# Kernel tuning notes

Measured on AMD Instinct MI355X. Metric: run time of the kernel, lower is better.

The kernel has to match this reference:

```python
import jax, jax.numpy as jnp
import numpy as np

N_NODES = 100000
N_EDGES = 3200000
N_GRAPHS = 64
IN_FEATS = 128
NUM_CLASSES = 10


def setup_inputs() -> dict:
    key = jax.random.key(0)
    ks = jax.random.split(key, 12)
    in_feat = jax.random.normal(ks[0], (N_NODES, IN_FEATS), dtype=jnp.float32)
    src = jax.random.randint(ks[1], (N_EDGES,), 0, N_NODES, dtype=jnp.int32)
    dst = jax.random.randint(ks[2], (N_EDGES,), 0, N_NODES, dtype=jnp.int32)
    graph_ids = jnp.sort(jax.random.randint(ks[3], (N_NODES,), 0, N_GRAPHS, dtype=jnp.int32))
    def glorot(k, fan_in, fan_out):
        s = jnp.sqrt(6.0 / (fan_in + fan_out))
        return jax.random.uniform(k, (fan_in, fan_out), jnp.float32, -s, s)
    W1 = glorot(ks[4], IN_FEATS, 64); b1 = jnp.zeros((64,), jnp.float32)
    W2 = glorot(ks[5], 64, 128);      b2 = jnp.zeros((128,), jnp.float32)
    W3 = glorot(ks[6], 128, 64);      b3 = jnp.zeros((64,), jnp.float32)
    Wd = glorot(ks[7], 64, NUM_CLASSES)
    bd = jnp.zeros((NUM_CLASSES,), jnp.float32)
    return {"in_feat": in_feat, "src": src, "dst": dst, "graph_ids": graph_ids,
            "W1": W1, "b1": b1, "W2": W2, "b2": b2, "W3": W3, "b3": b3,
            "Wd": Wd, "bd": bd}


def _graph_conv(h, src, dst, norm_src, norm_dst, W, b):
    # DGL GraphConv, norm='both': h' = D_in^{-1/2} A (D_out^{-1/2} h) W + b
    x = h * norm_src[:, None]
    m = jax.ops.segment_sum(x[src], dst, num_segments=N_NODES)
    m = m * norm_dst[:, None]
    return m @ W + b


def reference(in_feat, src, dst, graph_ids, W1, b1, W2, b2, W3, b3, Wd, bd):
    ones = jnp.ones((N_EDGES,), jnp.float32)
    deg_out = jax.ops.segment_sum(ones, src, num_segments=N_NODES)
    deg_in = jax.ops.segment_sum(ones, dst, num_segments=N_NODES)
    norm_src = jax.lax.rsqrt(jnp.clip(deg_out, 1.0))
    norm_dst = jax.lax.rsqrt(jnp.clip(deg_in, 1.0))

    h = jax.nn.relu(_graph_conv(in_feat, src, dst, norm_src, norm_dst, W1, b1))
    h = jax.nn.relu(_graph_conv(h, src, dst, norm_src, norm_dst, W2, b2))
    h = jax.nn.relu(_graph_conv(h, src, dst, norm_src, norm_dst, W3, b3))

    hg = jax.ops.segment_sum(h, graph_ids, num_segments=N_GRAPHS)  # [G, 64]
    hg = jnp.tanh(hg)
    return hg @ Wd + bd  # [G, num_classes]
```

## Files before the change

kernel.cpp:

```cpp
#include <hip/hip_runtime.h>
#include <hip/hip_bf16.h>


constexpr int NN = 100000;
constexpr int NE = 3200000;
constexpr int NG = 64;

constexpr int CBITS = 16;
constexpr int CHUNK = 1 << CBITS;
constexpr int NCHUNK = (NE + CHUNK - 1) / CHUNK;
constexpr int WORDS4 = NN / 8;

typedef __attribute__((ext_vector_type(8))) short short8;
typedef __attribute__((ext_vector_type(4))) float f32x4;
typedef __attribute__((ext_vector_type(2))) float f32x2;


__global__ __launch_bounds__(1024) void hist_kernel(
    const int* __restrict__ src, const int* __restrict__ dst,
    uint* __restrict__ pdst, uint* __restrict__ psrc,
    unsigned char* __restrict__ lrank) {
  __shared__ uint bins[WORDS4];
  for (int i = threadIdx.x; i < WORDS4; i += 1024) bins[i] = 0;
  __syncthreads();
  const int c = blockIdx.x;
  const int start = c << CBITS;
  const int end = min(start + CHUNK, NE);
  if (blockIdx.y == 0) {
    for (int i = start + threadIdx.x; i < end; i += 1024) {
      int n = dst[i];
      uint old = atomicAdd(&bins[n >> 3], 1u << ((n & 7) * 4));
      lrank[i] = (unsigned char)((old >> ((n & 7) * 4)) & 0xf);
    }
  } else {
    for (int i = start + threadIdx.x; i < end; i += 1024) {
      int n = src[i];
      atomicAdd(&bins[n >> 3], 1u << ((n & 7) * 4));
    }
  }
  __syncthreads();
  uint* pp = ((blockIdx.y == 0) ? pdst : psrc) + (size_t)c * WORDS4;
  for (int i = threadIdx.x; i < WORDS4; i += 1024) pp[i] = bins[i];
}


__global__ __launch_bounds__(256) void reduce2_kernel(
    const uint* __restrict__ pdst, const uint* __restrict__ psrc,
    unsigned char* __restrict__ Pb, int* __restrict__ deg_in,
    float* __restrict__ nd, float* __restrict__ ns, float* __restrict__ hg) {
  int w = blockIdx.x * 256 + threadIdx.x;
  uint run[8] = {0, 0, 0, 0, 0, 0, 0, 0};
  if (blockIdx.y == 0) {
    if (w >= WORDS4) return;
#pragma unroll 7
    for (int c = 0; c < NCHUNK; ++c) {
      uint lo = run[0] | (run[1] << 8) | (run[2] << 16) | (run[3] << 24);
      uint hi = run[4] | (run[5] << 8) | (run[6] << 16) | (run[7] << 24);
      ((uint2*)(Pb + (size_t)c * NN))[w] = make_uint2(lo, hi);
      uint v = pdst[(size_t)c * WORDS4 + w];
#pragma unroll
      for (int k = 0; k < 8; ++k) run[k] += (v >> (4 * k)) & 0xfu;
    }
    ((int4*)deg_in)[2 * w] = make_int4(run[0], run[1], run[2], run[3]);
    ((int4*)deg_in)[2 * w + 1] = make_int4(run[4], run[5], run[6], run[7]);
    float4 f0, f1;
    f0.x = rsqrtf(fmaxf((float)run[0], 1.f));
    f0.y = rsqrtf(fmaxf((float)run[1], 1.f));
    f0.z = rsqrtf(fmaxf((float)run[2], 1.f));
    f0.w = rsqrtf(fmaxf((float)run[3], 1.f));
    f1.x = rsqrtf(fmaxf((float)run[4], 1.f));
    f1.y = rsqrtf(fmaxf((float)run[5], 1.f));
    f1.z = rsqrtf(fmaxf((float)run[6], 1.f));
    f1.w = rsqrtf(fmaxf((float)run[7], 1.f));
    ((float4*)nd)[2 * w] = f0;
    ((float4*)nd)[2 * w + 1] = f1;
  } else {
    if (blockIdx.x == 0) {
      for (int k = threadIdx.x; k < 1024; k += 256)
        ((float4*)hg)[k] = make_float4(0.f, 0.f, 0.f, 0.f);
    }
    if (w >= WORDS4) return;
#pragma unroll 7
    for (int c = 0; c < NCHUNK; ++c) {
      uint v = psrc[(size_t)c * WORDS4 + w];
#pragma unroll
      for (int k = 0; k < 8; ++k) run[k] += (v >> (4 * k)) & 0xfu;
    }
    float4 f0, f1;
    f0.x = rsqrtf(fmaxf((float)run[0], 1.f));
    f0.y = rsqrtf(fmaxf((float)run[1], 1.f));
    f0.z = rsqrtf(fmaxf((float)run[2], 1.f));
    f0.w = rsqrtf(fmaxf((float)run[3], 1.f));
    f1.x = rsqrtf(fmaxf((float)run[4], 1.f));
    f1.y = rsqrtf(fmaxf((float)run[5], 1.f));
    f1.z = rsqrtf(fmaxf((float)run[6], 1.f));
    f1.w = rsqrtf(fmaxf((float)run[7], 1.f));
    ((float4*)ns)[2 * w] = f0;
    ((float4*)ns)[2 * w + 1] = f1;
  }
}


__device__ __forceinline__ uint pack_bf16(float a, float b) {
  uint ua = __float_as_uint(a), ub = __float_as_uint(b);
  ua = (ua + 0x7fffu + ((ua >> 16) & 1u)) >> 16;
  ub = (ub + 0x7fffu + ((ub >> 16) & 1u)) & 0xffff0000u;
  return ua | ub;
}

__device__ __forceinline__ ushort to_bf16(float a) {
  uint ua = __float_as_uint(a);
  return (ushort)((ua + 0x7fffu + ((ua >> 16) & 1u)) >> 16);
}

union U16 {
  uint4 u;
  short8 s;
};
__device__ __forceinline__ short8 as_short8(uint4 u) {
  U16 t;
  t.u = u;
  return t.s;
}

__device__ __forceinline__ f32x2 bf2(uint u) {
  f32x2 r;
  r.x = __uint_as_float(u << 16);
  r.y = __uint_as_float(u & 0xffff0000u);
  return r;
}

__device__ __forceinline__ void add8(f32x2* a, uint4 v) {
  a[0] += bf2(v.x);
  a[1] += bf2(v.y);
  a[2] += bf2(v.z);
  a[3] += bf2(v.w);
}


__global__ __launch_bounds__(256) void scan1t_kernel(
    const int* __restrict__ deg, int* __restrict__ row_off,
    int* __restrict__ bsums, int n, const float* __restrict__ W1,
    const float* __restrict__ W2, const float* __restrict__ W3,
    ushort* __restrict__ Wt1, ushort* __restrict__ Wt2,
    ushort* __restrict__ Wt3) {
  int gi = blockIdx.x * 256 + threadIdx.x;
  if (gi < 8192) {
    int nn = gi >> 7, k = gi & 127;
    Wt1[gi] = to_bf16(W1[k * 64 + nn]);
  } else if (gi < 16384) {
    int j = gi - 8192;
    int nn = j >> 6, k = j & 63;
    Wt2[j] = to_bf16(W2[k * 128 + nn]);
  } else if (gi < 24576) {
    int j = gi - 16384;
    int nn = j >> 7, k = j & 127;
    Wt3[j] = to_bf16(W3[k * 64 + nn]);
  }
  __shared__ int s[256];
  int t = threadIdx.x;
  int base = blockIdx.x * 1024 + t * 4;
  int v0 = 0, v1 = 0, v2 = 0, v3 = 0;
  if (base + 0 < n) v0 = deg[base + 0];
  if (base + 1 < n) v1 = deg[base + 1];
  if (base + 2 < n) v2 = deg[base + 2];
  if (base + 3 < n) v3 = deg[base + 3];
  int sum = v0 + v1 + v2 + v3;
  s[t] = sum;
  __syncthreads();
  for (int off = 1; off < 256; off <<= 1) {
    int x = (t >= off) ? s[t - off] : 0;
    __syncthreads();
    s[t] += x;
    __syncthreads();
  }
  int excl = s[t] - sum;
  if (t == 255) bsums[blockIdx.x] = s[255];
  if (base + 0 < n) row_off[base + 0] = excl;
  if (base + 1 < n) row_off[base + 1] = excl + v0;
  if (base + 2 < n) row_off[base + 2] = excl + v0 + v1;
  if (base + 3 < n) row_off[base + 3] = excl + v0 + v1 + v2;
}


__global__ __launch_bounds__(256) void scan23_kernel(
    int* __restrict__ row_off, const int* __restrict__ bsums, int nb, int n) {
  __shared__ int si[128], so[128];
  int t = threadIdx.x;
  if (t < 128) {
    int v = (t < nb) ? bsums[t] : 0;
    si[t] = v;
    so[t] = v;
  }
  __syncthreads();
  for (int off = 1; off < 128; off <<= 1) {
    int x = 0;
    if (t < 128 && t >= off) x = si[t - off];
    __syncthreads();
    if (t < 128) si[t] += x;
    __syncthreads();
  }
  int i = blockIdx.x * 256 + t;
  if (i < n) {
    int bk = i >> 10;
    row_off[i] += si[bk] - so[bk];
  }
  if (blockIdx.x == 0 && t == 0) row_off[n] = si[127];
}


__global__ __launch_bounds__(256) void fillg1_kernel(
    const int* __restrict__ src, const int* __restrict__ dst,
    const int* __restrict__ row_off, const unsigned char* __restrict__ Pb,
    const unsigned char* __restrict__ lrank, int* __restrict__ csr, int e,
    const float* __restrict__ A, const ushort* __restrict__ Wt,
    const float* __restrict__ scale, ushort* __restrict__ C, int n,
    int gblocks) {
  if (blockIdx.x < (uint)gblocks) {
    int wid = threadIdx.x >> 6, lane = threadIdx.x & 63;
    int r = lane & 15, quad = lane >> 4;
    int m16 = blockIdx.x * 64 + wid * 16;
    if (m16 >= n) return;
    int mc = min(m16 + r, n - 1);
    short8 a[4];
#pragma unroll
    for (int ks = 0; ks < 4; ++ks) {
      const float4* p =
          (const float4*)(A + (size_t)mc * 128 + ks * 32 + quad * 8);
      float4 x = p[0], y = p[1];
      uint4 u;
      u.x = pack_bf16(x.x, x.y);
      u.y = pack_bf16(x.z, x.w);
      u.z = pack_bf16(y.x, y.y);
      u.w = pack_bf16(y.z, y.w);
      a[ks] = as_short8(u);
    }
#pragma unroll
    for (int nt = 0; nt < 4; ++nt) {
      f32x4 acc = {0.f, 0.f, 0.f, 0.f};
#pragma unroll
      for (int ks = 0; ks < 4; ++ks) {
        short8 b = as_short8(*(const uint4*)(Wt + (size_t)(nt * 16 + r) * 128 +
                                             ks * 32 + quad * 8));
        acc = __builtin_amdgcn_mfma_f32_16x16x32_bf16(a[ks], b, acc, 0, 0, 0);
      }
#pragma unroll
      for (int reg = 0; reg < 4; ++reg) {
        int m = m16 + quad * 4 + reg;
        if (m < n)
          C[(size_t)m * 64 + nt * 16 + r] = to_bf16(acc[reg] * scale[m]);
      }
    }
  } else {
    int i = (blockIdx.x - gblocks) * 256 + threadIdx.x;
    if (i < e) {
      int d = dst[i];
      int c = i >> CBITS;
      int pos = row_off[d] + (int)Pb[(size_t)c * NN + d] + (int)lrank[i];
      csr[pos] = src[i];
    }
  }
}


__global__ __launch_bounds__(256) void gemm23_kernel(
    const ushort* __restrict__ m2, const ushort* __restrict__ Wt2,
    const float* __restrict__ b2, const float* __restrict__ ns,
    const ushort* __restrict__ Wt3, ushort* __restrict__ t3, int n) {
  __shared__ ushort sX[4][16][136];
  int wid = threadIdx.x >> 6, lane = threadIdx.x & 63;
  int r = lane & 15, quad = lane >> 4;
  int m16 = blockIdx.x * 64 + wid * 16;
  if (m16 >= n) return;
  int mc = min(m16 + r, n - 1);
  short8 a1[2];
#pragma unroll
  for (int ks = 0; ks < 2; ++ks)
    a1[ks] = as_short8(*(const uint4*)(m2 + (size_t)mc * 64 + ks * 32 + quad * 8));
  float nsv[4];
#pragma unroll
  for (int reg = 0; reg < 4; ++reg)
    nsv[reg] = ns[min(m16 + quad * 4 + reg, n - 1)];
#pragma unroll
  for (int nt = 0; nt < 8; ++nt) {
    f32x4 acc = {0.f, 0.f, 0.f, 0.f};
#pragma unroll
    for (int ks = 0; ks < 2; ++ks) {
      short8 b = as_short8(
          *(const uint4*)(Wt2 + (size_t)(nt * 16 + r) * 64 + ks * 32 + quad * 8));
      acc = __builtin_amdgcn_mfma_f32_16x16x32_bf16(a1[ks], b, acc, 0, 0, 0);
    }
    float bv = b2[nt * 16 + r];
#pragma unroll
    for (int reg = 0; reg < 4; ++reg) {
      float v = fmaxf(acc[reg] + bv, 0.f) * nsv[reg];
      sX[wid][quad * 4 + reg][nt * 16 + r] = to_bf16(v);
    }
  }
  short8 a2[4];
#pragma unroll
  for (int ks = 0; ks < 4; ++ks)
    a2[ks] = as_short8(*(const uint4*)(&sX[wid][r][ks * 32 + quad * 8]));
#pragma unroll
  for (int nt = 0; nt < 4; ++nt) {
    f32x4 acc = {0.f, 0.f, 0.f, 0.f};
#pragma unroll
    for (int ks = 0; ks < 4; ++ks) {
      short8 b = as_short8(
          *(const uint4*)(Wt3 + (size_t)(nt * 16 + r) * 128 + ks * 32 + quad * 8));
      acc = __builtin_amdgcn_mfma_f32_16x16x32_bf16(a2[ks], b, acc, 0, 0, 0);
    }
#pragma unroll
    for (int reg = 0; reg < 4; ++reg) {
      int m = m16 + quad * 4 + reg;
      if (m < n) t3[(size_t)m * 64 + nt * 16 + r] = to_bf16(acc[reg]);
    }
  }
}


__device__ __forceinline__ void gather2_bf16(const int* __restrict__ csr,
                                             const ushort* __restrict__ x,
                                             int rs, int rm, int re, int lane,
                                             f32x2* a0, f32x2* a1) {
  const int eg = lane >> 3;
  const int fl = lane & 7;
  for (int e0 = rs; e0 < re; e0 += 64) {
    int idx = e0 + lane;
    int sv = (idx < re) ? csr[idx] : 0;
    int cnt = re - e0;
    if (cnt > 64) cnt = 64;
    int c0 = rm - e0;
#pragma unroll
    for (int j = 0; j < 8; ++j) {
      int jb = j * 8;
      if (jb < cnt) {
        int s = __shfl(sv, jb + eg);
        uint4 v = *(const uint4*)(x + (size_t)s * 64 + fl * 8);
        if (jb + 8 > cnt) {
          uint mv = ((jb + eg) < cnt) ? 0xffffffffu : 0u;
          v.x &= mv; v.y &= mv; v.z &= mv; v.w &= mv;
        }
        if (jb + 8 <= c0) {
          add8(a0, v);
        } else if (jb >= c0) {
          add8(a1, v);
        } else {
          uint m0 = ((jb + eg) < c0) ? 0xffffffffu : 0u;
          uint4 v0;
          v0.x = v.x & m0; v0.y = v.y & m0; v0.z = v.z & m0; v0.w = v.w & m0;
          add8(a0, v0);
          v.x ^= v0.x; v.y ^= v0.y; v.z ^= v0.z; v.w ^= v0.w;
          add8(a1, v);
        }
      }
    }
  }
#pragma unroll
  for (int k = 0; k < 4; ++k) {
    a0[k].x += __shfl_xor(a0[k].x, 8);
    a0[k].x += __shfl_xor(a0[k].x, 16);
    a0[k].x += __shfl_xor(a0[k].x, 32);
    a0[k].y += __shfl_xor(a0[k].y, 8);
    a0[k].y += __shfl_xor(a0[k].y, 16);
    a0[k].y += __shfl_xor(a0[k].y, 32);
    a1[k].x += __shfl_xor(a1[k].x, 8);
    a1[k].x += __shfl_xor(a1[k].x, 16);
    a1[k].x += __shfl_xor(a1[k].x, 32);
    a1[k].y += __shfl_xor(a1[k].y, 8);
    a1[k].y += __shfl_xor(a1[k].y, 16);
    a1[k].y += __shfl_xor(a1[k].y, 32);
  }
}

#define ACC_SEL(k) ((eg == 0) ? a0[(k) >> 1][(k)&1] : a1[(k) >> 1][(k)&1])


__global__ __launch_bounds__(256) void agg1_kernel(
    const int* __restrict__ row_off, const int* __restrict__ csr,
    const ushort* __restrict__ t, const float* __restrict__ nd,
    const float* __restrict__ ns, const float* __restrict__ b,
    ushort* __restrict__ out, int n) {
  int wid = threadIdx.x >> 6, lane = threadIdx.x & 63;
  int n0 = blockIdx.x * 8 + wid * 2;
  int rs = row_off[n0], rm = row_off[n0 + 1], re = row_off[n0 + 2];
  f32x2 a0[4] = {{0, 0}, {0, 0}, {0, 0}, {0, 0}};
  f32x2 a1[4] = {{0, 0}, {0, 0}, {0, 0}, {0, 0}};
  gather2_bf16(csr, t, rs, rm, re, lane, a0, a1);
  int eg = lane >> 3, fl = lane & 7;
  if (eg < 2) {
    int node = n0 + eg;
    float ndv = nd[node], nsv = ns[node];
    const float4* bp = (const float4*)(b + fl * 8);
    float4 b0 = bp[0], b1v = bp[1];
    float o0 = fmaxf(ACC_SEL(0) * ndv + b0.x, 0.f) * nsv;
    float o1 = fmaxf(ACC_SEL(1) * ndv + b0.y, 0.f) * nsv;
    float o2 = fmaxf(ACC_SEL(2) * ndv + b0.z, 0.f) * nsv;
    float o3 = fmaxf(ACC_SEL(3) * ndv + b0.w, 0.f) * nsv;
    float o4 = fmaxf(ACC_SEL(4) * ndv + b1v.x, 0.f) * nsv;
    float o5 = fmaxf(ACC_SEL(5) * ndv + b1v.y, 0.f) * nsv;
    float o6 = fmaxf(ACC_SEL(6) * ndv + b1v.z, 0.f) * nsv;
    float o7 = fmaxf(ACC_SEL(7) * ndv + b1v.w, 0.f) * nsv;
    uint4 v;
    v.x = pack_bf16(o0, o1);
    v.y = pack_bf16(o2, o3);
    v.z = pack_bf16(o4, o5);
    v.w = pack_bf16(o6, o7);
    *(uint4*)(out + (size_t)node * 64 + fl * 8) = v;
  }
}


__global__ __launch_bounds__(256) void agg2_kernel(
    const int* __restrict__ row_off, const int* __restrict__ csr,
    const ushort* __restrict__ h1s, const float* __restrict__ nd,
    ushort* __restrict__ m2, int n) {
  int wid = threadIdx.x >> 6, lane = threadIdx.x & 63;
  int n0 = blockIdx.x * 8 + wid * 2;
  int rs = row_off[n0], rm = row_off[n0 + 1], re = row_off[n0 + 2];
  f32x2 a0[4] = {{0, 0}, {0, 0}, {0, 0}, {0, 0}};
  f32x2 a1[4] = {{0, 0}, {0, 0}, {0, 0}, {0, 0}};
  gather2_bf16(csr, h1s, rs, rm, re, lane, a0, a1);
  int eg = lane >> 3, fl = lane & 7;
  if (eg < 2) {
    int node = n0 + eg;
    float ndv = nd[node];
    uint4 v;
    v.x = pack_bf16(ACC_SEL(0) * ndv, ACC_SEL(1) * ndv);
    v.y = pack_bf16(ACC_SEL(2) * ndv, ACC_SEL(3) * ndv);
    v.z = pack_bf16(ACC_SEL(4) * ndv, ACC_SEL(5) * ndv);
    v.w = pack_bf16(ACC_SEL(6) * ndv, ACC_SEL(7) * ndv);
    *(uint4*)(m2 + (size_t)node * 64 + fl * 8) = v;
  }
}


__global__ __launch_bounds__(512) void agg3_kernel(
    const int* __restrict__ row_off, const int* __restrict__ csr,
    const ushort* __restrict__ t, const float* __restrict__ nd,
    const float* __restrict__ b, const int* __restrict__ gid,
    float* __restrict__ hg, int n) {
  __shared__ float sO[16][64];
  __shared__ int sG[16];
  __shared__ int uni;
  int wid = threadIdx.x >> 6, lane = threadIdx.x & 63;
  int n0 = blockIdx.x * 16 + wid * 2;
  int rs = row_off[n0], rm = row_off[n0 + 1], re = row_off[n0 + 2];
  f32x2 a0[4] = {{0, 0}, {0, 0}, {0, 0}, {0, 0}};
  f32x2 a1[4] = {{0, 0}, {0, 0}, {0, 0}, {0, 0}};
  gather2_bf16(csr, t, rs, rm, re, lane, a0, a1);
  int eg = lane >> 3, fl = lane & 7;
  if (eg < 2) {
    int node = n0 + eg;
    int row = wid * 2 + eg;
    float ndv = nd[node];
    const float4* bp = (const float4*)(b + fl * 8);
    float4 b0 = bp[0], b1v = bp[1];
    sO[row][fl * 8 + 0] = fmaxf(ACC_SEL(0) * ndv + b0.x, 0.f);
    sO[row][fl * 8 + 1] = fmaxf(ACC_SEL(1) * ndv + b0.y, 0.f);
    sO[row][fl * 8 + 2] = fmaxf(ACC_SEL(2) * ndv + b0.z, 0.f);
    sO[row][fl * 8 + 3] = fmaxf(ACC_SEL(3) * ndv + b0.w, 0.f);
    sO[row][fl * 8 + 4] = fmaxf(ACC_SEL(4) * ndv + b1v.x, 0.f);
    sO[row][fl * 8 + 5] = fmaxf(ACC_SEL(5) * ndv + b1v.y, 0.f);
    sO[row][fl * 8 + 6] = fmaxf(ACC_SEL(6) * ndv + b1v.z, 0.f);
    sO[row][fl * 8 + 7] = fmaxf(ACC_SEL(7) * ndv + b1v.w, 0.f);
  }
  if (lane == 0) sG[wid * 2] = gid[n0];
  if (lane == 8) sG[wid * 2 + 1] = gid[n0 + 1];
  __syncthreads();
  if (threadIdx.x == 0) {
    int g0 = sG[0], u = 1;
#pragma unroll
    for (int i = 1; i < 16; ++i) u &= (sG[i] == g0);
    uni = u;
  }
  __syncthreads();
  if (uni) {
    int r = threadIdx.x >> 6;
#pragma unroll
    for (int s = 8; s >= 1; s >>= 1) {
      if (r < s) sO[r][lane] += sO[r + s][lane];
      __syncthreads();
    }
    if (threadIdx.x < 64) atomicAdd(&hg[sG[0] * 64 + lane], sO[0][lane]);
  } else {
    atomicAdd(&hg[sG[wid * 2] * 64 + lane], sO[wid * 2][lane]);
    atomicAdd(&hg[sG[wid * 2 + 1] * 64 + lane], sO[wid * 2 + 1][lane]);
  }
}


__global__ __launch_bounds__(640) void readout_kernel(
    const float* __restrict__ hg, const float* __restrict__ Wd,
    const float* __restrict__ bd, float* __restrict__ out) {
  int t = threadIdx.x;
  int g = t / 10, c = t % 10;
  float o = bd[c];
#pragma unroll 8
  for (int k = 0; k < 64; ++k) o += tanhf(hg[g * 64 + k]) * Wd[k * 10 + c];
  out[t] = o;
}


extern "C" void kernel_launch(void* const* d_in, const int* in_sizes, int n_in,
                              void* d_out, int out_size, void* d_ws, size_t ws_size,
                              hipStream_t stream) {
  const float* in_feat = (const float*)d_in[0];
  const int* src = (const int*)d_in[1];
  const int* dst = (const int*)d_in[2];
  const int* gid = (const int*)d_in[3];
  const float* W1 = (const float*)d_in[4];
  const float* b1 = (const float*)d_in[5];
  const float* W2 = (const float*)d_in[6];
  const float* b2 = (const float*)d_in[7];
  const float* W3 = (const float*)d_in[8];
  const float* b3 = (const float*)d_in[9];
  const float* Wd = (const float*)d_in[10];
  const float* bd = (const float*)d_in[11];
  float* out = (float*)d_out;

  char* ws = (char*)d_ws;
  size_t o = 0;
  auto alloc = [&](size_t bytes) -> char* {
    char* p = ws + o;
    o = (o + bytes + 1023) & ~(size_t)1023;
    return p;
  };
  float* hg = (float*)alloc(NG * 64 * 4);
  int* deg_in = (int*)alloc(NN * 4);
  float* norm_src = (float*)alloc(NN * 4);
  float* norm_dst = (float*)alloc(NN * 4);
  int* row_off = (int*)alloc((NN + 1) * 4);
  int* bsums = (int*)alloc(512);
  ushort* Wt1 = (ushort*)alloc(64 * 128 * 2);
  ushort* Wt2 = (ushort*)alloc(128 * 64 * 2);
  ushort* Wt3 = (ushort*)alloc(64 * 128 * 2);
  int* csr = (int*)alloc((size_t)NE * 4);
  ushort* tbuf = (ushort*)alloc((size_t)NN * 64 * 2);
  ushort* h1s = (ushort*)alloc((size_t)NN * 64 * 2);
  ushort* m2 = (ushort*)alloc((size_t)NN * 64 * 2);
  (void)ws_size;

  char* ov = (char*)h1s;
  uint* pdst = (uint*)ov;
  uint* psrc = (uint*)(ov + 2457600);
  unsigned char* Pb = (unsigned char*)(ov + 4915200);
  unsigned char* lrank = (unsigned char*)(ov + 9830400);

  const int egrid = (NE + 255) / 256;
  const int ngrid = (NN + 255) / 256;
  const int sgrid = (NN + 1023) / 1024;
  const int wgrid2 = NN / 8;
  const int rgrid = (WORDS4 + 255) / 256;
  const int ggrid = (NN + 63) / 64;

  hist_kernel<<<dim3(NCHUNK, 2), 1024, 0, stream>>>(src, dst, pdst, psrc, lrank);
  reduce2_kernel<<<dim3(rgrid, 2), 256, 0, stream>>>(pdst, psrc, Pb, deg_in,
                                                     norm_dst, norm_src, hg);
  scan1t_kernel<<<sgrid, 256, 0, stream>>>(deg_in, row_off, bsums, NN, W1, W2,
                                           W3, Wt1, Wt2, Wt3);
  scan23_kernel<<<ngrid, 256, 0, stream>>>(row_off, bsums, sgrid, NN);
  fillg1_kernel<<<ggrid + egrid, 256, 0, stream>>>(
      src, dst, row_off, Pb, lrank, csr, NE, in_feat, Wt1, norm_src, tbuf, NN,
      ggrid);
  agg1_kernel<<<wgrid2, 256, 0, stream>>>(row_off, csr, tbuf, norm_dst,
                                          norm_src, b1, h1s, NN);
  agg2_kernel<<<wgrid2, 256, 0, stream>>>(row_off, csr, h1s, norm_dst, m2, NN);
  gemm23_kernel<<<ggrid, 256, 0, stream>>>(m2, Wt2, b2, norm_src, Wt3, tbuf, NN);
  agg3_kernel<<<NN / 16, 512, 0, stream>>>(row_off, csr, tbuf, norm_dst, b3,
                                           gid, hg, NN);
  readout_kernel<<<1, 640, 0, stream>>>(hg, Wd, bd, out);
}
```

Before: 430.8 us.

## Fuse layer-2 aggregation with layer-2/3 GEMMs into one kernel

Merges the agg2 gather kernel and the gemm23 MFMA kernel, so aggregated rows go into shared memory and the 64->128->64 transforms run in the same block. Blocks grow to 512 threads covering 16 nodes, with each wave computing one 16-column output tile. This removes the m2 intermediate round-trip through global memory and one kernel launch. In exchange it adds two block-wide barriers, and half the waves sit idle during the second GEMM.

```diff
diff --git a/kernel.cpp b/kernel.cpp
--- a/kernel.cpp
+++ b/kernel.cpp
@@ -258,62 +258,6 @@
       int c = i >> CBITS;
       int pos = row_off[d] + (int)Pb[(size_t)c * NN + d] + (int)lrank[i];
       csr[pos] = src[i];
-    }
-  }
-}
-
-
-__global__ __launch_bounds__(256) void gemm23_kernel(
-    const ushort* __restrict__ m2, const ushort* __restrict__ Wt2,
-    const float* __restrict__ b2, const float* __restrict__ ns,
-    const ushort* __restrict__ Wt3, ushort* __restrict__ t3, int n) {
-  __shared__ ushort sX[4][16][136];
-  int wid = threadIdx.x >> 6, lane = threadIdx.x & 63;
-  int r = lane & 15, quad = lane >> 4;
-  int m16 = blockIdx.x * 64 + wid * 16;
-  if (m16 >= n) return;
-  int mc = min(m16 + r, n - 1);
-  short8 a1[2];
-#pragma unroll
-  for (int ks = 0; ks < 2; ++ks)
-    a1[ks] = as_short8(*(const uint4*)(m2 + (size_t)mc * 64 + ks * 32 + quad * 8));
-  float nsv[4];
-#pragma unroll
-  for (int reg = 0; reg < 4; ++reg)
-    nsv[reg] = ns[min(m16 + quad * 4 + reg, n - 1)];
-#pragma unroll
-  for (int nt = 0; nt < 8; ++nt) {
-    f32x4 acc = {0.f, 0.f, 0.f, 0.f};
-#pragma unroll
-    for (int ks = 0; ks < 2; ++ks) {
-      short8 b = as_short8(
-          *(const uint4*)(Wt2 + (size_t)(nt * 16 + r) * 64 + ks * 32 + quad * 8));
-      acc = __builtin_amdgcn_mfma_f32_16x16x32_bf16(a1[ks], b, acc, 0, 0, 0);
-    }
-    float bv = b2[nt * 16 + r];
-#pragma unroll
-    for (int reg = 0; reg < 4; ++reg) {
-      float v = fmaxf(acc[reg] + bv, 0.f) * nsv[reg];
-      sX[wid][quad * 4 + reg][nt * 16 + r] = to_bf16(v);
-    }
-  }
-  short8 a2[4];
-#pragma unroll
-  for (int ks = 0; ks < 4; ++ks)
-    a2[ks] = as_short8(*(const uint4*)(&sX[wid][r][ks * 32 + quad * 8]));
-#pragma unroll
-  for (int nt = 0; nt < 4; ++nt) {
-    f32x4 acc = {0.f, 0.f, 0.f, 0.f};
-#pragma unroll
-    for (int ks = 0; ks < 4; ++ks) {
-      short8 b = as_short8(
-          *(const uint4*)(Wt3 + (size_t)(nt * 16 + r) * 128 + ks * 32 + quad * 8));
-      acc = __builtin_amdgcn_mfma_f32_16x16x32_bf16(a2[ks], b, acc, 0, 0, 0);
-    }
-#pragma unroll
-    for (int reg = 0; reg < 4; ++reg) {
-      int m = m16 + quad * 4 + reg;
-      if (m < n) t3[(size_t)m * 64 + nt * 16 + r] = to_bf16(acc[reg]);
     }
   }
 }
@@ -411,12 +355,16 @@
 }
 
 
-__global__ __launch_bounds__(256) void agg2_kernel(
+__global__ __launch_bounds__(512) void agg2g23_kernel(
     const int* __restrict__ row_off, const int* __restrict__ csr,
     const ushort* __restrict__ h1s, const float* __restrict__ nd,
-    ushort* __restrict__ m2, int n) {
+    const ushort* __restrict__ Wt2, const float* __restrict__ b2,
+    const float* __restrict__ ns, const ushort* __restrict__ Wt3,
+    ushort* __restrict__ t3, int n) {
+  __shared__ ushort sM[16][72];
+  __shared__ ushort sX[16][136];
   int wid = threadIdx.x >> 6, lane = threadIdx.x & 63;
-  int n0 = blockIdx.x * 8 + wid * 2;
+  int n0 = blockIdx.x * 16 + wid * 2;
   int rs = row_off[n0], rm = row_off[n0 + 1], re = row_off[n0 + 2];
   f32x2 a0[4] = {{0, 0}, {0, 0}, {0, 0}, {0, 0}};
   f32x2 a1[4] = {{0, 0}, {0, 0}, {0, 0}, {0, 0}};
@@ -424,13 +372,58 @@
   int eg = lane >> 3, fl = lane & 7;
   if (eg < 2) {
     int node = n0 + eg;
+    int row = wid * 2 + eg;
     float ndv = nd[node];
     uint4 v;
     v.x = pack_bf16(ACC_SEL(0) * ndv, ACC_SEL(1) * ndv);
     v.y = pack_bf16(ACC_SEL(2) * ndv, ACC_SEL(3) * ndv);
     v.z = pack_bf16(ACC_SEL(4) * ndv, ACC_SEL(5) * ndv);
     v.w = pack_bf16(ACC_SEL(6) * ndv, ACC_SEL(7) * ndv);
-    *(uint4*)(m2 + (size_t)node * 64 + fl * 8) = v;
+    *(uint4*)(&sM[row][fl * 8]) = v;
+  }
+  __syncthreads();
+  const int tb = blockIdx.x * 16;
+  int r = lane & 15, quad = lane >> 4;
+  {
+    int nt = wid;
+    short8 af[2];
+#pragma unroll
+    for (int ks = 0; ks < 2; ++ks)
+      af[ks] = as_short8(*(const uint4*)(&sM[r][ks * 32 + quad * 8]));
+    f32x4 acc = {0.f, 0.f, 0.f, 0.f};
+#pragma unroll
+    for (int ks = 0; ks < 2; ++ks) {
+      short8 b = as_short8(
+          *(const uint4*)(Wt2 + (size_t)(nt * 16 + r) * 64 + ks * 32 + quad * 8));
+      acc = __builtin_amdgcn_mfma_f32_16x16x32_bf16(af[ks], b, acc, 0, 0, 0);
+    }
+    float bv = b2[nt * 16 + r];
+#pragma unroll
+    for (int reg = 0; reg < 4; ++reg) {
+      int m = tb + quad * 4 + reg;
+      float v = fmaxf(acc[reg] + bv, 0.f) * ns[m];
+      sX[quad * 4 + reg][nt * 16 + r] = to_bf16(v);
+    }
+  }
+  __syncthreads();
+  if (wid < 4) {
+    int nt = wid;
+    short8 af[4];
+#pragma unroll
+    for (int ks = 0; ks < 4; ++ks)
+      af[ks] = as_short8(*(const uint4*)(&sX[r][ks * 32 + quad * 8]));
+    f32x4 acc = {0.f, 0.f, 0.f, 0.f};
+#pragma unroll
+    for (int ks = 0; ks < 4; ++ks) {
+      short8 b = as_short8(
+          *(const uint4*)(Wt3 + (size_t)(nt * 16 + r) * 128 + ks * 32 + quad * 8));
+      acc = __builtin_amdgcn_mfma_f32_16x16x32_bf16(af[ks], b, acc, 0, 0, 0);
+    }
+#pragma unroll
+    for (int reg = 0; reg < 4; ++reg) {
+      int m = tb + quad * 4 + reg;
+      t3[(size_t)m * 64 + nt * 16 + r] = to_bf16(acc[reg]);
+    }
   }
 }
 
@@ -538,8 +531,9 @@
   int* csr = (int*)alloc((size_t)NE * 4);
   ushort* tbuf = (ushort*)alloc((size_t)NN * 64 * 2);
   ushort* h1s = (ushort*)alloc((size_t)NN * 64 * 2);
-  ushort* m2 = (ushort*)alloc((size_t)NN * 64 * 2);
+  ushort* sp2 = (ushort*)alloc((size_t)NN * 64 * 2);
   (void)ws_size;
+  (void)sp2;
 
   char* ov = (char*)h1s;
   uint* pdst = (uint*)ov;
@@ -565,8 +559,8 @@
       ggrid);
   agg1_kernel<<<wgrid2, 256, 0, stream>>>(row_off, csr, tbuf, norm_dst,
                                           norm_src, b1, h1s, NN);
-  agg2_kernel<<<wgrid2, 256, 0, stream>>>(row_off, csr, h1s, norm_dst, m2, NN);
-  gemm23_kernel<<<ggrid, 256, 0, stream>>>(m2, Wt2, b2, norm_src, Wt3, tbuf, NN);
+  agg2g23_kernel<<<NN / 16, 512, 0, stream>>>(row_off, csr, h1s, norm_dst, Wt2,
+                                              b2, norm_src, Wt3, tbuf, NN);
   agg3_kernel<<<NN / 16, 512, 0, stream>>>(row_off, csr, tbuf, norm_dst, b3,
                                            gid, hg, NN);
   readout_kernel<<<1, 640, 0, stream>>>(hg, Wd, bd, out);
```

New measurement: 423.3 us, median of 2. No clear change (-1.7%).
